# Kernel tuning notes

Measured on AMD Instinct MI355X. Metric: run time of the kernel, lower is better.

The kernel has to match this reference:

```python
import jax, jax.numpy as jnp
import numpy as np

B, S, D = 4, 2048, 2048
NH, NKV = 16, 4
HD = D // NH  # 128


def setup_inputs() -> dict:
    key = jax.random.key(0)
    ks = jax.random.split(key, 6)
    sd = 1.0 / np.sqrt(D)
    return {
        "x": jax.random.normal(ks[0], (B, S, D), jnp.float32),
        "cos": jax.random.normal(ks[1], (1, 1, S, HD), jnp.float32),
        "sin": jax.random.normal(ks[2], (1, 1, S, HD), jnp.float32),
        "wq_w": jax.random.normal(ks[3], (D, D), jnp.float32) * sd,
        "wk_w": jax.random.normal(ks[4], (NKV * HD, D), jnp.float32) * sd,
        "wv_w": jax.random.normal(ks[5], (NKV * HD, D), jnp.float32) * sd,
        "start_pos": 0,
    }


def _rotate_half(t):
    h = t.shape[-1] // 2
    return jnp.concatenate([-t[..., h:], t[..., :h]], axis=-1)


def reference(x, cos, sin, wq_w, wk_w, wv_w, start_pos):
    b, s, d = x.shape
    n_rep = NH // NKV
    q = (x @ wq_w.T).reshape(b, s, NH, HD).transpose(0, 2, 1, 3)      # [b,H,s,hd]
    k = (x @ wk_w.T).reshape(b, s, NKV, HD).transpose(0, 2, 1, 3)     # [b,Hk,s,hd]
    v = (x @ wv_w.T).reshape(b, s, NKV, HD).transpose(0, 2, 1, 3)
    # rotary
    q = q * cos + _rotate_half(q) * sin
    k = k * cos + _rotate_half(k) * sin
    # repeat_kv
    k = jnp.repeat(k, n_rep, axis=1)   # [b,H,s,hd]
    v = jnp.repeat(v, n_rep, axis=1)
    scores = jnp.einsum("bhqd,bhkd->bhqk", q, k) / jnp.sqrt(jnp.float32(HD))
    causal = jnp.tril(jnp.ones((s, s), dtype=bool))
    scores = jnp.where(causal, scores, jnp.float32(-jnp.inf))
    w = jax.nn.softmax(scores, axis=-1)
    out = jnp.einsum("bhqk,bhkd->bhqd", w, v)
    return out.transpose(0, 2, 1, 3).reshape(b, s, d)
```

## Files before the change

kernel.cpp:

```cpp
#include <hip/hip_runtime.h>
#include <hip/hip_bf16.h>
#include <math.h>

#define B_ 4
#define S_ 2048
#define D_ 2048
#define NH_ 16
#define NKV_ 4
#define HD_ 128

typedef short bf16x8 __attribute__((ext_vector_type(8)));
typedef float f32x4 __attribute__((ext_vector_type(4)));
typedef unsigned u32x4 __attribute__((ext_vector_type(4)));
typedef __hip_bfloat16 bf16;

#define ASYNC_CP16(gp, lp)                                                    \
  __builtin_amdgcn_global_load_lds(                                           \
      (const __attribute__((address_space(1))) unsigned int*)(gp),            \
      (__attribute__((address_space(3))) unsigned int*)(lp), 16, 0, 0)

__global__ __launch_bounds__(256) void cvt_kernel(const float* __restrict__ in,
                                                  bf16* __restrict__ out, int n4) {
  int i = blockIdx.x * 256 + threadIdx.x;
  if (i >= n4) return;
  float4 v = ((const float4*)in)[i];
  union { ushort4 u; bf16 h[4]; } o;
  o.h[0] = __float2bfloat16(v.x);
  o.h[1] = __float2bfloat16(v.y);
  o.h[2] = __float2bfloat16(v.z);
  o.h[3] = __float2bfloat16(v.w);
  ((ushort4*)out)[i] = o.u;
}

__global__ __launch_bounds__(256) void gemm_qkv(
    const bf16* __restrict__ A, const bf16* __restrict__ W,
    bf16* __restrict__ qr, bf16* __restrict__ kr, bf16* __restrict__ vlin,
    const float* __restrict__ cosp, const float* __restrict__ sinp,
    float qscale) {
  __shared__ __align__(16) bf16 As[128 * 64];
  __shared__ __align__(16) bf16 Bs[128 * 64];
  const int tid = threadIdx.x;
  const int lane = tid & 63, wave = tid >> 6;
  const int wm = (wave & 1) * 64, wn = (wave >> 1) * 64;
  const int m0 = blockIdx.x * 128;
  const int hblk = blockIdx.y;
  const int n0 = hblk * 128;
  const int quad = lane >> 4, c = lane & 15;
  const int K = 2048;

  f32x4 acc[4][4] = {};

  const int sr = lane >> 3;
  const int sg = lane & 7;
  const int gc = (sg ^ sr) * 8;
  const bf16* Ap = A + (size_t)(m0 + wave * 32 + sr) * K + gc;
  const bf16* Bp = W + (size_t)(n0 + wave * 32 + sr) * K + gc;

  for (int kb = 0; kb < K; kb += 64) {
    __syncthreads();
#pragma unroll
    for (int i = 0; i < 4; i++) {
      ASYNC_CP16(Ap + (size_t)(i * 8) * K + kb, &As[(wave * 32 + i * 8) * 64]);
      ASYNC_CP16(Bp + (size_t)(i * 8) * K + kb, &Bs[(wave * 32 + i * 8) * 64]);
    }
    __syncthreads();
#pragma unroll
    for (int kk = 0; kk < 2; kk++) {
      const int slot = ((kk * 4 + quad) ^ (c & 7)) * 8;
      bf16x8 af[4], bfr[4];
#pragma unroll
      for (int t = 0; t < 4; t++) {
        af[t]  = *(const bf16x8*)(&As[(wm + t * 16 + c) * 64 + slot]);
        bfr[t] = *(const bf16x8*)(&Bs[(wn + t * 16 + c) * 64 + slot]);
      }
#pragma unroll
      for (int mt = 0; mt < 4; mt++)
#pragma unroll
        for (int nt = 0; nt < 4; nt++)
          acc[mt][nt] = __builtin_amdgcn_mfma_f32_16x16x32_bf16(
              af[mt], bfr[nt], acc[mt][nt], 0, 0, 0);
    }
  }

  if (hblk >= 20) {
    const int colb = (hblk - 20) * 128 + wn;
#pragma unroll
    for (int mt = 0; mt < 4; mt++)
#pragma unroll
      for (int reg = 0; reg < 4; reg++) {
        int m = m0 + wm + mt * 16 + quad * 4 + reg;
        bf16* row = vlin + (size_t)m * (NKV_ * HD_) + colb;
#pragma unroll
        for (int nt = 0; nt < 4; nt++)
          row[nt * 16 + c] = __float2bfloat16(acc[mt][nt][reg]);
      }
  } else {
    float* Sc = (float*)As;
    __syncthreads();
    if (wave >= 2) {
#pragma unroll
      for (int mt = 0; mt < 4; mt++)
#pragma unroll
        for (int reg = 0; reg < 4; reg++) {
          int lr = wm + mt * 16 + quad * 4 + reg;
#pragma unroll
          for (int nt = 0; nt < 4; nt++)
            Sc[lr * 64 + nt * 16 + c] = acc[mt][nt][reg];
        }
    }
    __syncthreads();
    if (wave < 2) {
      const float scale = (hblk < 16) ? qscale : 1.0f;
#pragma unroll
      for (int mt = 0; mt < 4; mt++)
#pragma unroll
        for (int reg = 0; reg < 4; reg++) {
          int lr = wm + mt * 16 + quad * 4 + reg;
          int m = m0 + lr;
          int b = m >> 11, s = m & 2047;
          const float* cr = cosp + s * HD_;
          const float* sn = sinp + s * HD_;
          bf16* orow = (hblk < 16)
              ? qr + ((size_t)(b * NH_ + hblk) * S_ + s) * HD_
              : kr + ((size_t)(b * NKV_ + (hblk - 16)) * S_ + s) * HD_;
#pragma unroll
          for (int nt = 0; nt < 4; nt++) {
            int d1 = nt * 16 + c, d2 = d1 + 64;
            float q1 = acc[mt][nt][reg];
            float q2 = Sc[lr * 64 + d1];
            float o1 = (q1 * cr[d1] - q2 * sn[d1]) * scale;
            float o2 = (q2 * cr[d2] + q1 * sn[d2]) * scale;
            orow[d1] = __float2bfloat16(o1);
            orow[d2] = __float2bfloat16(o2);
          }
        }
    }
  }
}

__global__ __launch_bounds__(256) void v_transpose(const bf16* __restrict__ in,
                                                   int instride,
                                                   bf16* __restrict__ out) {
  __shared__ __align__(16) bf16 tile[64][HD_ + 8];
  int bidx = blockIdx.x;
  int st = bidx & 31;
  int kv = (bidx >> 5) & 3;
  int b = bidx >> 7;
  int s0 = st * 64;
  int t = threadIdx.x;
  {
    int row = t >> 2;
    int colb = (t & 3) * 32;
#pragma unroll
    for (int i = 0; i < 4; i++) {
      int col = colb + i * 8;
      *(uint4*)(&tile[row][col]) = *(const uint4*)(
          &in[(size_t)(b * S_ + s0 + row) * instride + kv * HD_ + col]);
    }
  }
  __syncthreads();
  int sl = t & 63, hb = t >> 6;
#pragma unroll
  for (int i = 0; i < 32; i++) {
    int hd = i * 4 + hb;
    out[((size_t)(b * NKV_ + kv) * HD_ + hd) * S_ + s0 + sl] = tile[sl][hd];
  }
}

__device__ __forceinline__ void attn_step2(
    const bf16* __restrict__ Ks, const bf16* __restrict__ Vs,
    bf16* __restrict__ PsA, bf16* __restrict__ PsB,
    const bf16x8* qfA, const bf16x8* qfB, f32x4* oA, f32x4* oB,
    float& mA, float& lA, float& mB, float& lB,
    bool diagA, bool diagB, int kb, int qbA, int quad, int c) {
  f32x4 sA[4] = {}, sB[4] = {};
#pragma unroll
  for (int kt = 0; kt < 4; kt++) {
    const int slot = ((kt * 4 + quad) ^ (c & 7)) * 8;
#pragma unroll
    for (int mt = 0; mt < 4; mt++) {
      bf16x8 kf = *(const bf16x8*)(&Ks[(mt * 16 + c) * 128 + slot]);
      sA[mt] = __builtin_amdgcn_mfma_f32_16x16x32_bf16(kf, qfA[kt], sA[mt], 0, 0, 0);
      sB[mt] = __builtin_amdgcn_mfma_f32_16x16x32_bf16(kf, qfB[kt], sB[mt], 0, 0, 0);
    }
  }
  if (diagA) {
    const int qg = qbA + c;
#pragma unroll
    for (int mt = 0; mt < 4; mt++)
#pragma unroll
      for (int r = 0; r < 4; r++)
        if (kb + mt * 16 + quad * 4 + r > qg) sA[mt][r] = -INFINITY;
  }
  if (diagB) {
    const int qg = qbA + 16 + c;
#pragma unroll
    for (int mt = 0; mt < 4; mt++)
#pragma unroll
      for (int r = 0; r < 4; r++)
        if (kb + mt * 16 + quad * 4 + r > qg) sB[mt][r] = -INFINITY;
  }

#define SOFTMAX_PACK(sacc, m_i, l_i, o, Psw)                                  \
  do {                                                                        \
    f32x4 mx4 = __builtin_elementwise_max(                                    \
        __builtin_elementwise_max(sacc[0], sacc[1]),                          \
        __builtin_elementwise_max(sacc[2], sacc[3]));                         \
    float mx = fmaxf(fmaxf(mx4[0], mx4[1]), fmaxf(mx4[2], mx4[3]));          \
    mx = fmaxf(mx, __shfl_xor(mx, 16, 64));                                   \
    mx = fmaxf(mx, __shfl_xor(mx, 32, 64));                                   \
    if (!__all(mx - m_i <= 8.0f)) {                                           \
      const float mnew = fmaxf(m_i, mx);                                      \
      const float alpha = exp2f(m_i - mnew);                                  \
      m_i = mnew;                                                             \
      l_i *= alpha;                                                           \
      f32x4 av;                                                               \
      av[0] = __shfl(alpha, quad * 4 + 0, 64);                                \
      av[1] = __shfl(alpha, quad * 4 + 1, 64);                                \
      av[2] = __shfl(alpha, quad * 4 + 2, 64);                                \
      av[3] = __shfl(alpha, quad * 4 + 3, 64);                                \
      _Pragma("unroll")                                                       \
      for (int nt = 0; nt < 8; nt++) o[nt] *= av;                             \
    }                                                                         \
    const f32x4 mn4 = {m_i, m_i, m_i, m_i};                                   \
    f32x4 rs4 = {0.f, 0.f, 0.f, 0.f};                                         \
    _Pragma("unroll")                                                         \
    for (int mt = 0; mt < 4; mt++) {                                          \
      f32x4 e = sacc[mt] - mn4;                                               \
      f32x4 p;                                                                \
      p[0] = exp2f(e[0]); p[1] = exp2f(e[1]);                                 \
      p[2] = exp2f(e[2]); p[3] = exp2f(e[3]);                                 \
      rs4 += p;                                                               \
      u32x4 u = __builtin_bit_cast(u32x4, p) + 0x8000u;                       \
      uint2 pk;                                                               \
      pk.x = __builtin_amdgcn_perm(u[1], u[0], 0x07060302u);                  \
      pk.y = __builtin_amdgcn_perm(u[3], u[2], 0x07060302u);                  \
      const int pslot = mt * 2 + (quad >> 1);                                 \
      *(uint2*)(&Psw[c * 64 + ((pslot ^ (c & 7)) << 3) + (quad & 1) * 4]) = pk; \
    }                                                                         \
    float rs = (rs4[0] + rs4[1]) + (rs4[2] + rs4[3]);                         \
    rs += __shfl_xor(rs, 16, 64);                                             \
    rs += __shfl_xor(rs, 32, 64);                                             \
    l_i += rs;                                                                \
  } while (0)

  SOFTMAX_PACK(sA, mA, lA, oA, PsA);
  SOFTMAX_PACK(sB, mB, lB, oB, PsB);
#undef SOFTMAX_PACK

#pragma unroll
  for (int kk = 0; kk < 2; kk++) {
    const int psl = (((kk * 4 + quad) ^ (c & 7)) << 3);
    bf16x8 pfA = *(const bf16x8*)(&PsA[c * 64 + psl]);
    bf16x8 pfB = *(const bf16x8*)(&PsB[c * 64 + psl]);
    const int slot = ((kk * 4 + quad) ^ (c & 7)) * 8;
#pragma unroll
    for (int nt = 0; nt < 8; nt++) {
      bf16x8 vf = *(const bf16x8*)(&Vs[(nt * 16 + c) * 64 + slot]);
      oA[nt] = __builtin_amdgcn_mfma_f32_16x16x32_bf16(pfA, vf, oA[nt], 0, 0, 0);
      oB[nt] = __builtin_amdgcn_mfma_f32_16x16x32_bf16(pfB, vf, oB[nt], 0, 0, 0);
    }
  }
}

__global__ __launch_bounds__(256, 2) void attn_kernel(const bf16* __restrict__ Q,
                                                      const bf16* __restrict__ Kr,
                                                      const bf16* __restrict__ Vt,
                                                      float* __restrict__ O) {
  __shared__ __align__(16) bf16 Ks[2][64 * 128];
  __shared__ __align__(16) bf16 Vs[2][128 * 64];
  __shared__ __align__(16) bf16 Ps[4][2][16 * 64];

  const int tid = threadIdx.x, lane = tid & 63, wave = tid >> 6;
  const int quad = lane >> 4, c = lane & 15;
  const int j = blockIdx.x;
  const int bh = blockIdx.y;
  const int b = bh >> 4, h = bh & 15, kv = h >> 2;
  bf16* PsA = &Ps[wave][0][0];
  bf16* PsB = &Ps[wave][1][0];

  const bf16* kbase = Kr + (size_t)(b * NKV_ + kv) * S_ * HD_;
  const bf16* vbase = Vt + (size_t)(b * NKV_ + kv) * HD_ * S_;

  int koff[4], voff;
  {
    const int kl = lane >> 4;
    const int ks = lane & 15;
#pragma unroll
    for (int i = 0; i < 4; i++) {
      int r = wave * 16 + i * 4 + kl;
      koff[i] = r * HD_ + ((ks ^ (r & 7)) * 8);
    }
    const int vl = lane >> 3;
    const int vs = lane & 7;
    voff = (wave * 32 + vl) * S_ + ((vs ^ (vl & 7)) * 8);
  }

#define STAGE(kb_, buf_)                                                      \
  do {                                                                        \
    _Pragma("unroll")                                                         \
    for (int i_ = 0; i_ < 4; i_++) {                                          \
      ASYNC_CP16(kbase + (size_t)(kb_) * HD_ + koff[i_],                      \
                 &Ks[buf_][(wave * 16 + i_ * 4) * 128]);                      \
      ASYNC_CP16(vbase + (kb_) + voff + (size_t)(i_ * 8) * S_,                \
                 &Vs[buf_][(wave * 32 + i_ * 8) * 64]);                       \
    }                                                                         \
  } while (0)

#pragma unroll 1
  for (int pass = 0; pass < 2; ++pass) {
    const int jj = pass ? (15 - j) : j;
    const int q0 = jj * 128;
    const int qb = q0 + wave * 32;
    const int nsteps = 2 * jj + 2;

    bf16x8 qfA[4], qfB[4];
    {
      const bf16* qpA = Q + ((size_t)(b * NH_ + h) * S_ + qb + c) * HD_;
      const bf16* qpB = qpA + (size_t)16 * HD_;
#pragma unroll
      for (int kt = 0; kt < 4; kt++) {
        qfA[kt] = *(const bf16x8*)(qpA + kt * 32 + quad * 8);
        qfB[kt] = *(const bf16x8*)(qpB + kt * 32 + quad * 8);
      }
    }
    f32x4 oA[8] = {}, oB[8] = {};
    float mA = -INFINITY, lA = 0.f, mB = -INFINITY, lB = 0.f;

    __syncthreads();
    STAGE(0, 0);
    int cur = 0;

#pragma unroll 1
    for (int it = 0; it < nsteps; ++it) {
      const int kb = it * 64;
      __syncthreads();
      if (it + 1 < nsteps) STAGE((it + 1) * 64, cur ^ 1);
      if (kb <= qb + 31)
        attn_step2(&Ks[cur][0], &Vs[cur][0], PsA, PsB, qfA, qfB, oA, oB,
                   mA, lA, mB, lB, kb + 63 > qb, kb + 63 > qb + 16,
                   kb, qb, quad, c);
      cur ^= 1;
    }

    float* obase = O + (size_t)b * S_ * D_ + (size_t)h * HD_;
    {
      float inv[4];
#pragma unroll
      for (int r = 0; r < 4; r++) inv[r] = 1.0f / __shfl(lA, quad * 4 + r, 64);
#pragma unroll
      for (int nt = 0; nt < 8; nt++)
#pragma unroll
        for (int r = 0; r < 4; r++)
          obase[(size_t)(qb + quad * 4 + r) * D_ + nt * 16 + c] = oA[nt][r] * inv[r];
    }
    {
      float inv[4];
#pragma unroll
      for (int r = 0; r < 4; r++) inv[r] = 1.0f / __shfl(lB, quad * 4 + r, 64);
#pragma unroll
      for (int nt = 0; nt < 8; nt++)
#pragma unroll
        for (int r = 0; r < 4; r++)
          obase[(size_t)(qb + 16 + quad * 4 + r) * D_ + nt * 16 + c] = oB[nt][r] * inv[r];
    }
  }
#undef STAGE
}

extern "C" void kernel_launch(void* const* d_in, const int* in_sizes, int n_in,
                              void* d_out, int out_size, void* d_ws, size_t ws_size,
                              hipStream_t stream) {
  const float* x    = (const float*)d_in[0];
  const float* cosp = (const float*)d_in[1];
  const float* sinp = (const float*)d_in[2];
  const float* wq   = (const float*)d_in[3];
  const float* wk   = (const float*)d_in[4];
  const float* wv   = (const float*)d_in[5];
  float* out = (float*)d_out;

  char* ws = (char*)d_ws;
  const size_t MB = 1024 * 1024;
  bf16* xb    = (bf16*)(ws + 0);
  bf16* wqkvb = (bf16*)(ws + 32 * MB);
  bf16* qr    = (bf16*)(ws + 44 * MB);
  bf16* kr    = (bf16*)(ws + 76 * MB);
  bf16* vlin  = (bf16*)(ws + 84 * MB);
  bf16* vt    = (bf16*)(ws + 92 * MB);

  cvt_kernel<<<16384, 256, 0, stream>>>(x, xb, 4194304);
  cvt_kernel<<<4096, 256, 0, stream>>>(wq, wqkvb, 1048576);
  cvt_kernel<<<1024, 256, 0, stream>>>(wk, wqkvb + 4194304, 262144);
  cvt_kernel<<<1024, 256, 0, stream>>>(wv, wqkvb + 5242880, 262144);

  const float qscale = 1.4426950408889634f / 11.313708498984761f;
  gemm_qkv<<<dim3(64, 24), 256, 0, stream>>>(xb, wqkvb, qr, kr, vlin,
                                             cosp, sinp, qscale);

  v_transpose<<<512, 256, 0, stream>>>(vlin, NKV_ * HD_, vt);

  attn_kernel<<<dim3(8, 64), 256, 0, stream>>>(qr, kr, vt, out);
}
```

Measured before the change: 380.8 us.

## Triple-buffer QKV GEMM with 256x128 tiles and merge weight conversions

The QKV projection GEMM moves from a single-buffered 128x128 tile with 256 threads to a 256x128 tile with 512 threads. It uses a three-stage LDS ring: async global-to-LDS copies for tile t+2 are issued between the MFMA phases of tile t, with vmcnt-based waits and a single barrier per iteration. The grid order is swapped so that blocks sharing the same M rows sit next to each other, and the three separate weight conversion launches are merged into one kernel. The aim is to hide global load latency and cut launch overhead, at the cost of about 147KB of LDS, which limits occupancy to one block per CU.

```diff
diff --git a/kernel.cpp b/kernel.cpp
--- a/kernel.cpp
+++ b/kernel.cpp
@@ -32,47 +32,86 @@
   ((ushort4*)out)[i] = o.u;
 }
 
-__global__ __launch_bounds__(256) void gemm_qkv(
+__global__ __launch_bounds__(256) void cvt_w_kernel(const float* __restrict__ wq,
+                                                    const float* __restrict__ wk,
+                                                    const float* __restrict__ wv,
+                                                    bf16* __restrict__ out) {
+  int i = blockIdx.x * 256 + threadIdx.x;
+  const float4* src; int off;
+  if (i < 1048576)      { src = (const float4*)wq; off = i; }
+  else if (i < 1310720) { src = (const float4*)wk; off = i - 1048576; }
+  else                  { src = (const float4*)wv; off = i - 1310720; }
+  float4 v = src[off];
+  union { ushort4 u; bf16 h[4]; } o;
+  o.h[0] = __float2bfloat16(v.x);
+  o.h[1] = __float2bfloat16(v.y);
+  o.h[2] = __float2bfloat16(v.z);
+  o.h[3] = __float2bfloat16(v.w);
+  ((ushort4*)out)[i] = o.u;
+}
+
+__global__ __launch_bounds__(512, 2) void gemm_qkv(
     const bf16* __restrict__ A, const bf16* __restrict__ W,
     bf16* __restrict__ qr, bf16* __restrict__ kr, bf16* __restrict__ vlin,
     const float* __restrict__ cosp, const float* __restrict__ sinp,
     float qscale) {
-  __shared__ __align__(16) bf16 As[128 * 64];
-  __shared__ __align__(16) bf16 Bs[128 * 64];
+  __shared__ __align__(16) bf16 As[3][256 * 64];
+  __shared__ __align__(16) bf16 Bs[3][128 * 64];
   const int tid = threadIdx.x;
   const int lane = tid & 63, wave = tid >> 6;
-  const int wm = (wave & 1) * 64, wn = (wave >> 1) * 64;
-  const int m0 = blockIdx.x * 128;
-  const int hblk = blockIdx.y;
+  const int wm = (wave >> 1) * 64, wn = (wave & 1) * 64;
+  const int hblk = blockIdx.x;
+  const int m0 = blockIdx.y * 256;
   const int n0 = hblk * 128;
   const int quad = lane >> 4, c = lane & 15;
   const int K = 2048;
+  const int T = K / 64;
 
   f32x4 acc[4][4] = {};
 
-  const int sr = lane >> 3;
-  const int sg = lane & 7;
-  const int gc = (sg ^ sr) * 8;
-  const bf16* Ap = A + (size_t)(m0 + wave * 32 + sr) * K + gc;
-  const bf16* Bp = W + (size_t)(n0 + wave * 32 + sr) * K + gc;
-
-  for (int kb = 0; kb < K; kb += 64) {
-    __syncthreads();
-#pragma unroll
-    for (int i = 0; i < 4; i++) {
-      ASYNC_CP16(Ap + (size_t)(i * 8) * K + kb, &As[(wave * 32 + i * 8) * 64]);
-      ASYNC_CP16(Bp + (size_t)(i * 8) * K + kb, &Bs[(wave * 32 + i * 8) * 64]);
-    }
-    __syncthreads();
-#pragma unroll
-    for (int kk = 0; kk < 2; kk++) {
-      const int slot = ((kk * 4 + quad) ^ (c & 7)) * 8;
+  const int srow = wave * 8 + (lane >> 3);
+  const int gcol = ((lane & 7) ^ ((lane >> 3) & 7)) * 8;
+  const bf16* Aptr = A + (size_t)(m0 + srow) * K + gcol;
+  const bf16* Bptr = W + (size_t)(n0 + srow) * K + gcol;
+
+#define STAGE_A(kb_, buf_, i_)                                                \
+  ASYNC_CP16(Aptr + (size_t)(i_) * 64 * K + (kb_),                            \
+             &As[buf_][((i_) * 64 + wave * 8) * 64])
+#define STAGE_B(kb_, buf_, i_)                                                \
+  ASYNC_CP16(Bptr + (size_t)(i_) * 64 * K + (kb_),                            \
+             &Bs[buf_][((i_) * 64 + wave * 8) * 64])
+
+  {
+#pragma unroll
+    for (int i = 0; i < 4; i++) STAGE_A(0, 0, i);
+#pragma unroll
+    for (int i = 0; i < 2; i++) STAGE_B(0, 0, i);
+#pragma unroll
+    for (int i = 0; i < 4; i++) STAGE_A(64, 1, i);
+#pragma unroll
+    for (int i = 0; i < 2; i++) STAGE_B(64, 1, i);
+    asm volatile("s_waitcnt vmcnt(6)" ::: "memory");
+    __builtin_amdgcn_s_barrier();
+    __builtin_amdgcn_sched_barrier(0);
+  }
+
+  int cur = 0, stg = 2;
+#pragma unroll 1
+  for (int t = 0; t < T; ++t) {
+    const bf16* Asc = &As[cur][0];
+    const bf16* Bsc = &Bs[cur][0];
+    const bool st = (t + 2) < T;
+    const size_t kb2 = (size_t)(t + 2) * 64;
+
+    {
+      const int slot = (quad ^ (c & 7)) * 8;
       bf16x8 af[4], bfr[4];
 #pragma unroll
-      for (int t = 0; t < 4; t++) {
-        af[t]  = *(const bf16x8*)(&As[(wm + t * 16 + c) * 64 + slot]);
-        bfr[t] = *(const bf16x8*)(&Bs[(wn + t * 16 + c) * 64 + slot]);
+      for (int q4 = 0; q4 < 4; q4++) {
+        af[q4]  = *(const bf16x8*)(&Asc[(wm + q4 * 16 + c) * 64 + slot]);
+        bfr[q4] = *(const bf16x8*)(&Bsc[(wn + q4 * 16 + c) * 64 + slot]);
       }
+      if (st) { STAGE_A(kb2, stg, 0); STAGE_A(kb2, stg, 1); STAGE_A(kb2, stg, 2); }
 #pragma unroll
       for (int mt = 0; mt < 4; mt++)
 #pragma unroll
@@ -80,7 +119,36 @@
           acc[mt][nt] = __builtin_amdgcn_mfma_f32_16x16x32_bf16(
               af[mt], bfr[nt], acc[mt][nt], 0, 0, 0);
     }
-  }
+    {
+      const int slot = ((4 + quad) ^ (c & 7)) * 8;
+      bf16x8 af[4], bfr[4];
+#pragma unroll
+      for (int q4 = 0; q4 < 4; q4++) {
+        af[q4]  = *(const bf16x8*)(&Asc[(wm + q4 * 16 + c) * 64 + slot]);
+        bfr[q4] = *(const bf16x8*)(&Bsc[(wn + q4 * 16 + c) * 64 + slot]);
+      }
+      if (st) { STAGE_A(kb2, stg, 3); STAGE_B(kb2, stg, 0); STAGE_B(kb2, stg, 1); }
+#pragma unroll
+      for (int mt = 0; mt < 4; mt++)
+#pragma unroll
+        for (int nt = 0; nt < 4; nt++)
+          acc[mt][nt] = __builtin_amdgcn_mfma_f32_16x16x32_bf16(
+              af[mt], bfr[nt], acc[mt][nt], 0, 0, 0);
+    }
+
+    if (t + 1 < T) {
+      if (st) asm volatile("s_waitcnt vmcnt(6)" ::: "memory");
+      else    asm volatile("s_waitcnt vmcnt(0)" ::: "memory");
+      __builtin_amdgcn_s_barrier();
+      __builtin_amdgcn_sched_barrier(0);
+    }
+    cur = (cur == 2) ? 0 : cur + 1;
+    stg = (stg == 2) ? 0 : stg + 1;
+  }
+#undef STAGE_A
+#undef STAGE_B
+
+  __syncthreads();
 
   if (hblk >= 20) {
     const int colb = (hblk - 20) * 128 + wn;
@@ -95,9 +163,8 @@
           row[nt * 16 + c] = __float2bfloat16(acc[mt][nt][reg]);
       }
   } else {
-    float* Sc = (float*)As;
-    __syncthreads();
-    if (wave >= 2) {
+    float* Sc = (float*)&As[0][0];
+    if (wn) {
 #pragma unroll
       for (int mt = 0; mt < 4; mt++)
 #pragma unroll
@@ -109,7 +176,7 @@
         }
     }
     __syncthreads();
-    if (wave < 2) {
+    if (!wn) {
       const float scale = (hblk < 16) ? qscale : 1.0f;
 #pragma unroll
       for (int mt = 0; mt < 4; mt++)
@@ -389,12 +456,10 @@
   bf16* vt    = (bf16*)(ws + 92 * MB);
 
   cvt_kernel<<<16384, 256, 0, stream>>>(x, xb, 4194304);
-  cvt_kernel<<<4096, 256, 0, stream>>>(wq, wqkvb, 1048576);
-  cvt_kernel<<<1024, 256, 0, stream>>>(wk, wqkvb + 4194304, 262144);
-  cvt_kernel<<<1024, 256, 0, stream>>>(wv, wqkvb + 5242880, 262144);
+  cvt_w_kernel<<<6144, 256, 0, stream>>>(wq, wk, wv, wqkvb);
 
   const float qscale = 1.4426950408889634f / 11.313708498984761f;
-  gemm_qkv<<<dim3(64, 24), 256, 0, stream>>>(xb, wqkvb, qr, kr, vlin,
+  gemm_qkv<<<dim3(24, 32), 512, 0, stream>>>(xb, wqkvb, qr, kr, vlin,
                                              cosp, sinp, qscale);
 
   v_transpose<<<512, 256, 0, stream>>>(vlin, NKV_ * HD_, vt);
```

Measured after the change: 381.2 us. About the same (+0.1%).
